# Kernel optimization log

Hardware: AMD Instinct MI355X
Metric: run time of the kernel (lower is better)

The kernel has to match this reference:

```python
import jax, jax.numpy as jnp
import numpy as np


def _prelu(x, a):
    return jnp.where(x >= 0, x, a * x)


def _conv1x1(x, w, b, a):
    # x: [N,C,H,W], w: [O,C], b: [O] -> PReLU(conv1x1(x))
    y = jnp.einsum('oc,nchw->nohw', w, x) + b[None, :, None, None]
    return _prelu(y, a)


def setup_inputs() -> dict:
    key = jax.random.key(0)
    ks = jax.random.split(key, 8)
    N, C, H, W = 4, 128, 64, 64
    Cr = C // 2  # reduction=2
    sC = 1.0 / np.sqrt(C)
    x = jax.random.normal(ks[0], (N, C, H, W), dtype=jnp.float32)
    w1 = jax.random.normal(ks[1], (Cr, C), dtype=jnp.float32) * sC
    b1 = jnp.zeros((Cr,), dtype=jnp.float32)
    a1 = jnp.asarray(0.25, dtype=jnp.float32)  # PReLU (single shared slope)
    w2 = jax.random.normal(ks[2], (Cr, C), dtype=jnp.float32) * sC
    b2 = jnp.zeros((Cr,), dtype=jnp.float32)
    a2 = jnp.asarray(0.25, dtype=jnp.float32)
    wa = jax.random.normal(ks[3], (C, C), dtype=jnp.float32) * sC
    ba = jnp.zeros((C,), dtype=jnp.float32)
    aa = jnp.asarray(0.25, dtype=jnp.float32)
    return {"x": x, "w1": w1, "b1": b1, "a1": a1,
            "w2": w2, "b2": b2, "a2": a2,
            "wa": wa, "ba": ba, "aa": aa}


def reference(x, w1, b1, a1, w2, b2, a2, wa, ba, aa):
    N, C, H, W = x.shape
    HW = H * W
    e1 = _conv1x1(x, w1, b1, a1).reshape(N, -1, HW)   # [N,Cr,HW]
    e2 = _conv1x1(x, w2, b2, a2).reshape(N, -1, HW)   # [N,Cr,HW]
    asm = _conv1x1(x, wa, ba, aa).reshape(N, C, HW)   # [N,C,HW]
    # ksize=1: per-channel outer products summed over channels == single contraction
    score = jnp.einsum('nci,ncj->nij', e1, e2)        # [N,HW,HW]
    score = jax.nn.softmax(score, axis=2)
    out = jnp.einsum('nij,ncj->nci', score, asm)      # [N,C,HW]
    return out.reshape(N, C, H, W)
```

## Files before the change

### kernel.cpp

```cpp
#include <hip/hip_runtime.h>
#include <hip/hip_bf16.h>
#include <stdint.h>


typedef float   f32x16 __attribute__((ext_vector_type(16)));
typedef __bf16  bf16x8 __attribute__((ext_vector_type(8)));
typedef __bf16  bf16x2 __attribute__((ext_vector_type(2)));
typedef unsigned int u32x4 __attribute__((ext_vector_type(4)));
typedef unsigned int u32x2 __attribute__((ext_vector_type(2)));

#define L2E 1.4426950408889634f
#define NSHIFT (-12.0f * L2E)

#define Q_OFF   (0u)
#define K_OFF   (2u << 20)
#define V_OFF   (4u << 20)
#define DEN_OFF (8u << 20)
#define XTH_OFF ((8u << 20) + (1u << 19))
#define XTL_OFF (XTH_OFF + (4u << 20))
#define WH_OFF  (XTL_OFF + (4u << 20))
#define WL_OFF  (WH_OFF + (1u << 16))
#define OP_OFF  XTH_OFF

__device__ inline unsigned short f2bf(float f) {
  unsigned u = __builtin_bit_cast(unsigned, f);
  return (unsigned short)((u + 0x7FFFu + ((u >> 16) & 1u)) >> 16);
}
__device__ inline float bf2f(unsigned short h) {
  unsigned u = ((unsigned)h) << 16;
  return __builtin_bit_cast(float, u);
}

__device__ inline void gld_lds16(const void* g, void* l) {
  __builtin_amdgcn_global_load_lds(
      (const __attribute__((address_space(1))) unsigned*)g,
      (__attribute__((address_space(3))) unsigned*)l, 16, 0, 0);
}

__global__ __launch_bounds__(256) void transpose_kernel(
    const float* __restrict__ x, char* __restrict__ ws) {
  int bid = blockIdx.x;
  int n = bid >> 7, rem = bid & 127;
  int c0 = (rem >> 6) * 64, s0 = (rem & 63) * 64;
  int tid = threadIdx.x;
  __shared__ float tl[64][65];
  const float* xb = x + (size_t)n * 128 * 4096;
#pragma unroll
  for (int i = 0; i < 16; ++i) {
    int cl = (tid >> 6) * 16 + i;
    tl[cl][tid & 63] = xb[(size_t)(c0 + cl) * 4096 + s0 + (tid & 63)];
  }
  __syncthreads();
  char* XH = ws + XTH_OFF + (size_t)n * (4096 * 256);
  char* XL = ws + XTL_OFF + (size_t)n * (4096 * 256);
#pragma unroll
  for (int it = 0; it < 2; ++it) {
    int sl = (tid >> 3) + it * 32;
    int c8 = (tid & 7) * 8;
    unsigned short uh[8], ul[8];
#pragma unroll
    for (int i = 0; i < 8; ++i) {
      float v = tl[c8 + i][sl];
      unsigned short h = f2bf(v);
      uh[i] = h;
      ul[i] = f2bf(v - bf2f(h));
    }
    u32x4 ph, pl;
    ph.x = ((unsigned)uh[1] << 16) | uh[0]; ph.y = ((unsigned)uh[3] << 16) | uh[2];
    ph.z = ((unsigned)uh[5] << 16) | uh[4]; ph.w = ((unsigned)uh[7] << 16) | uh[6];
    pl.x = ((unsigned)ul[1] << 16) | ul[0]; pl.y = ((unsigned)ul[3] << 16) | ul[2];
    pl.z = ((unsigned)ul[5] << 16) | ul[4]; pl.w = ((unsigned)ul[7] << 16) | ul[6];
    size_t off = (size_t)(s0 + sl) * 256 + c0 * 2 + (tid & 7) * 16;
    *(u32x4*)(XH + off) = ph;
    *(u32x4*)(XL + off) = pl;
  }
}

__global__ void wcast_kernel(const float* __restrict__ w1, const float* __restrict__ w2,
                             const float* __restrict__ wa, char* __restrict__ ws) {
  int idx = blockIdx.x * 256 + threadIdx.x;
  unsigned short* WH = (unsigned short*)(ws + WH_OFF);
  unsigned short* WL = (unsigned short*)(ws + WL_OFF);
#pragma unroll
  for (int r = 0; r < 4; ++r) {
    int i = r * 8192 + idx;
    int oc = i >> 7, c = i & 127;
    float v = oc < 64 ? w1[oc * 128 + c]
            : (oc < 128 ? w2[(oc - 64) * 128 + c] : wa[(oc - 128) * 128 + c]);
    unsigned short h = f2bf(v);
    WH[i] = h;
    WL[i] = f2bf(v - bf2f(h));
  }
}

__global__ __launch_bounds__(256) void conv_kernel(
    char* __restrict__ ws,
    const float* __restrict__ b1, const float* __restrict__ a1,
    const float* __restrict__ b2, const float* __restrict__ a2,
    const float* __restrict__ ba, const float* __restrict__ aa) {
  int bid = blockIdx.x;
  int n = bid >> 7, st = bid & 127;
  int sb = st * 32;
  int tid = threadIdx.x;
  int wid = tid >> 6, lane = tid & 63, l31 = lane & 31, hi = lane >> 5;
  const char* XH = ws + XTH_OFF + (size_t)n * (4096 * 256);
  const char* XL = ws + XTL_OFF + (size_t)n * (4096 * 256);
  const char* WH = ws + WH_OFF;
  const char* WL = ws + WL_OFF;
  int oc0 = wid * 64;

  f32x16 acc[2];
  acc[0] = 0.f; acc[1] = 0.f;
#pragma unroll
  for (int c0 = 0; c0 < 8; ++c0) {
    size_t xo = (size_t)(sb + l31) * 256 + c0 * 32 + hi * 16;
    bf16x8 xh = *(const bf16x8*)(XH + xo);
    bf16x8 xl = *(const bf16x8*)(XL + xo);
#pragma unroll
    for (int mb = 0; mb < 2; ++mb) {
      size_t wo = (size_t)(oc0 + mb * 32 + l31) * 256 + c0 * 32 + hi * 16;
      bf16x8 wh = *(const bf16x8*)(WH + wo);
      bf16x8 wl = *(const bf16x8*)(WL + wo);
      acc[mb] = __builtin_amdgcn_mfma_f32_32x32x16_bf16(wh, xh, acc[mb], 0, 0, 0);
      acc[mb] = __builtin_amdgcn_mfma_f32_32x32x16_bf16(wh, xl, acc[mb], 0, 0, 0);
      acc[mb] = __builtin_amdgcn_mfma_f32_32x32x16_bf16(wl, xh, acc[mb], 0, 0, 0);
    }
  }

  __shared__ float tl[2][64][33];
  char* Qw = ws + Q_OFF + (size_t)n * (4096 * 64 * 2);
  char* Kw = ws + K_OFF + (size_t)n * (4096 * 64 * 2);
  unsigned short* Vw = (unsigned short*)(ws + V_OFF) + (size_t)n * 128 * 4096;

  if (wid < 2) {
    const float* bb = wid ? b2 : b1;
    float slope = wid ? a2[0] : a1[0];
#pragma unroll
    for (int mb = 0; mb < 2; ++mb)
#pragma unroll
      for (int reg = 0; reg < 16; ++reg) {
        int row = mb * 32 + (reg & 3) + 8 * (reg >> 2) + 4 * hi;
        float y = acc[mb][reg] + bb[row];
        y = fmaxf(y, 0.f) + slope * fminf(y, 0.f);
        tl[wid][row][l31] = y;
      }
  } else {
    float slope = aa[0];
#pragma unroll
    for (int mb = 0; mb < 2; ++mb)
#pragma unroll
      for (int reg = 0; reg < 16; ++reg) {
        int dv = (wid - 2) * 64 + mb * 32 + (reg & 3) + 8 * (reg >> 2) + 4 * hi;
        float y = acc[mb][reg] + ba[dv];
        y = fmaxf(y, 0.f) + slope * fminf(y, 0.f);
        Vw[(size_t)dv * 4096 + sb + l31] = f2bf(y);
      }
  }
  __syncthreads();
  if (wid < 2) {
    char* Og = wid ? Kw : Qw;
#pragma unroll
    for (int it = 0; it < 4; ++it) {
      int sl = (lane >> 3) + it * 8;
      unsigned short u[8];
#pragma unroll
      for (int i = 0; i < 8; ++i) u[i] = f2bf(tl[wid][(lane & 7) * 8 + i][sl]);
      u32x4 pv;
      pv.x = ((unsigned)u[1] << 16) | u[0]; pv.y = ((unsigned)u[3] << 16) | u[2];
      pv.z = ((unsigned)u[5] << 16) | u[4]; pv.w = ((unsigned)u[7] << 16) | u[6];
      *(u32x4*)(Og + (size_t)(sb + sl) * 128 + (lane & 7) * 16) = pv;
    }
  }
}

__global__ __launch_bounds__(256, 2) void attn_kernel(char* __restrict__ ws) {
  int bid = blockIdx.x;
  int batch   = (bid >> 1) & 3;
  int quarter = (bid >> 3) & 3;
  int qtile   = ((bid >> 5) << 1) | (bid & 1);
  int tid = threadIdx.x;
  int wid = tid >> 6, lane = tid & 63, l31 = lane & 31, hi = lane >> 5;

  const char* Qb = ws + Q_OFF + (size_t)batch * (4096 * 64 * 2);
  const char* Kb = ws + K_OFF + (size_t)batch * (4096 * 64 * 2);
  const char* Vb = ws + V_OFF + (size_t)batch * (128 * 4096 * 2);

  __shared__ char kbuf[2][64 * 128];
  __shared__ char vbuf[2][128 * 128];

  int q0 = qtile * 128 + wid * 32;

  bf16x8 qf[4];
#pragma unroll
  for (int d0 = 0; d0 < 4; ++d0)
    qf[d0] = *(const bf16x8*)(Qb + (size_t)(q0 + l31) * 128 + d0 * 32 + hi * 16);

  f32x16 oacc[4];
#pragma unroll
  for (int i = 0; i < 4; ++i) oacc[i] = 0.f;
  float den = 0.f;

  int t0 = quarter * 16;

  auto stage = [&](int b, int tile) {
    int kv0 = tile * 64;
#pragma unroll
    for (int i = 0; i < 2; ++i) {
      int base = wid * 2048 + i * 1024;
      int L = base + (lane << 4);
      int r = L >> 7, sl = (L >> 4) & 7;
      const char* src = Kb + (size_t)(kv0 + r) * 128 + ((sl ^ (r & 7)) << 4);
      gld_lds16(src, &kbuf[b][base]);
    }
#pragma unroll
    for (int i = 0; i < 4; ++i) {
      int base = wid * 4096 + i * 1024;
      int L = base + (lane << 4);
      int r = L >> 7, sl = (L >> 4) & 7;
      const char* src = Vb + (size_t)r * 8192 + kv0 * 2 + ((sl ^ (r & 7)) << 4);
      gld_lds16(src, &vbuf[b][base]);
    }
  };

  stage(0, t0);
  __syncthreads();
  int cur = 0;

  for (int t = 0; t < 16; ++t) {
    if (t + 1 < 16) stage(cur ^ 1, t0 + t + 1);

    f32x16 sacc[2];
    sacc[0] = 0.f; sacc[1] = 0.f;
#pragma unroll
    for (int kb = 0; kb < 2; ++kb) {
      int r = kb * 32 + l31;
#pragma unroll
      for (int d0 = 0; d0 < 4; ++d0) {
        bf16x8 kf = *(const bf16x8*)(&kbuf[cur][r * 128 + (((d0 * 2 + hi) ^ (r & 7)) << 4)]);
        sacc[kb] = __builtin_amdgcn_mfma_f32_32x32x16_bf16(kf, qf[d0], sacc[kb], 0, 0, 0);
      }
    }

    float p[2][16];
#pragma unroll
    for (int kb = 0; kb < 2; ++kb)
#pragma unroll
      for (int i = 0; i < 16; ++i) {
        float e = exp2f(fmaf(sacc[kb][i], L2E, NSHIFT));
        p[kb][i] = e;
        den += e;
      }

    unsigned pk[2][8];
#pragma unroll
    for (int kb = 0; kb < 2; ++kb)
#pragma unroll
      for (int m = 0; m < 8; ++m) {
        bf16x2 bp = { (__bf16)p[kb][2 * m], (__bf16)p[kb][2 * m + 1] };
        pk[kb][m] = __builtin_bit_cast(unsigned, bp);
      }

#pragma unroll
    for (int kc = 0; kc < 4; ++kc) {
      const int kb = kc >> 1, bs = (kc & 1) * 4;
      u32x2 r0 = __builtin_amdgcn_permlane32_swap(pk[kb][bs + 0], pk[kb][bs + 2],
                                                  false, false);
      u32x2 r1 = __builtin_amdgcn_permlane32_swap(pk[kb][bs + 1], pk[kb][bs + 3],
                                                  false, false);
      u32x4 pu = {r0.x, r1.x, r0.y, r1.y};
      bf16x8 pf = __builtin_bit_cast(bf16x8, pu);
#pragma unroll
      for (int dvb = 0; dvb < 4; ++dvb) {
        int r = dvb * 32 + l31;
        bf16x8 vf = *(const bf16x8*)(&vbuf[cur][r * 128 + (((kc * 2 + hi) ^ (r & 7)) << 4)]);
        oacc[dvb] = __builtin_amdgcn_mfma_f32_32x32x16_bf16(vf, pf, oacc[dvb], 0, 0, 0);
      }
    }

    __syncthreads();
    cur ^= 1;
  }

  float* OP = (float*)(ws + OP_OFF) +
              (size_t)((batch * 32 + qtile) * 4 + quarter) * 128 * 128;
  int qloc = wid * 32 + l31;
#pragma unroll
  for (int dvb = 0; dvb < 4; ++dvb)
#pragma unroll
    for (int reg = 0; reg < 16; ++reg) {
      int dv = dvb * 32 + (reg & 3) + 8 * (reg >> 2) + 4 * hi;
      OP[dv * 128 + qloc] = oacc[dvb][reg];
    }
  float dtot = den + __shfl_xor(den, 32, 64);
  if (hi == 0) {
    float* DEN = (float*)(ws + DEN_OFF) +
                 (size_t)((batch * 32 + qtile) * 4 + quarter) * 128;
    DEN[qloc] = dtot;
  }
}

__global__ __launch_bounds__(256) void combine_kernel(const char* __restrict__ ws,
                                                      float* __restrict__ out) {
  int idx = blockIdx.x * 256 + threadIdx.x;
  int n = idx >> 19;
  int dv = (idx >> 12) & 127;
  int s = idx & 4095;
  int qt = s >> 7, ql = s & 127;
  const float* OP = (const float*)(ws + OP_OFF);
  const float* DEN = (const float*)(ws + DEN_OFF);
  size_t pb = (size_t)((n * 32 + qt) * 4);
  float num = 0.f, den = 0.f;
#pragma unroll
  for (int h = 0; h < 4; ++h) {
    num += OP[((pb + h) * 128 + dv) * 128 + ql];
    den += DEN[(pb + h) * 128 + ql];
  }
  out[idx] = num / den;
}

extern "C" void kernel_launch(void* const* d_in, const int* in_sizes, int n_in,
                              void* d_out, int out_size, void* d_ws, size_t ws_size,
                              hipStream_t stream) {
  (void)in_sizes; (void)n_in; (void)out_size; (void)ws_size;
  const float* x  = (const float*)d_in[0];
  const float* w1 = (const float*)d_in[1];
  const float* b1 = (const float*)d_in[2];
  const float* a1 = (const float*)d_in[3];
  const float* w2 = (const float*)d_in[4];
  const float* b2 = (const float*)d_in[5];
  const float* a2 = (const float*)d_in[6];
  const float* wa = (const float*)d_in[7];
  const float* ba = (const float*)d_in[8];
  const float* aa = (const float*)d_in[9];
  char* ws = (char*)d_ws;
  float* out = (float*)d_out;

  transpose_kernel<<<dim3(512), dim3(256), 0, stream>>>(x, ws);
  wcast_kernel<<<dim3(32), dim3(256), 0, stream>>>(w1, w2, wa, ws);
  conv_kernel<<<dim3(512), dim3(256), 0, stream>>>(ws, b1, a1, b2, a2, ba, aa);
  attn_kernel<<<dim3(512), dim3(256), 0, stream>>>(ws);
  combine_kernel<<<dim3(8192), dim3(256), 0, stream>>>(ws, out);
}
```

Baseline: 73.20 us.

## Fuse transpose into conv, split attention KV eightways, drop softmax shift

Removes the separate transpose kernel: the conv kernel now loads x tiles into LDS and does the bf16 hi/lo split inline. The log2(e) scale is folded into Q during conv, so the attention kernel can use raw exp2 with no fixed shift. Attention is split into 8 KV chunks over 1024 blocks with occupancy hint 3, s_setprio around MFMA groups, and bf16 partial outputs that the combine kernel sums. This cuts launches, intermediate traffic and exp work, but loses the overflow guard from the shift and stores partial outputs at bf16 precision.

```diff
diff --git a/kernel.cpp b/kernel.cpp
--- a/kernel.cpp
+++ b/kernel.cpp
@@ -10,17 +10,14 @@
 typedef unsigned int u32x2 __attribute__((ext_vector_type(2)));
 
 #define L2E 1.4426950408889634f
-#define NSHIFT (-12.0f * L2E)
 
 #define Q_OFF   (0u)
 #define K_OFF   (2u << 20)
 #define V_OFF   (4u << 20)
 #define DEN_OFF (8u << 20)
-#define XTH_OFF ((8u << 20) + (1u << 19))
-#define XTL_OFF (XTH_OFF + (4u << 20))
-#define WH_OFF  (XTL_OFF + (4u << 20))
+#define WH_OFF  ((8u << 20) + (1u << 19))
 #define WL_OFF  (WH_OFF + (1u << 16))
-#define OP_OFF  XTH_OFF
+#define OP_OFF  (9u << 20)
 
 __device__ inline unsigned short f2bf(float f) {
   unsigned u = __builtin_bit_cast(unsigned, f);
@@ -35,45 +32,6 @@
   __builtin_amdgcn_global_load_lds(
       (const __attribute__((address_space(1))) unsigned*)g,
       (__attribute__((address_space(3))) unsigned*)l, 16, 0, 0);
-}
-
-__global__ __launch_bounds__(256) void transpose_kernel(
-    const float* __restrict__ x, char* __restrict__ ws) {
-  int bid = blockIdx.x;
-  int n = bid >> 7, rem = bid & 127;
-  int c0 = (rem >> 6) * 64, s0 = (rem & 63) * 64;
-  int tid = threadIdx.x;
-  __shared__ float tl[64][65];
-  const float* xb = x + (size_t)n * 128 * 4096;
-#pragma unroll
-  for (int i = 0; i < 16; ++i) {
-    int cl = (tid >> 6) * 16 + i;
-    tl[cl][tid & 63] = xb[(size_t)(c0 + cl) * 4096 + s0 + (tid & 63)];
-  }
-  __syncthreads();
-  char* XH = ws + XTH_OFF + (size_t)n * (4096 * 256);
-  char* XL = ws + XTL_OFF + (size_t)n * (4096 * 256);
-#pragma unroll
-  for (int it = 0; it < 2; ++it) {
-    int sl = (tid >> 3) + it * 32;
-    int c8 = (tid & 7) * 8;
-    unsigned short uh[8], ul[8];
-#pragma unroll
-    for (int i = 0; i < 8; ++i) {
-      float v = tl[c8 + i][sl];
-      unsigned short h = f2bf(v);
-      uh[i] = h;
-      ul[i] = f2bf(v - bf2f(h));
-    }
-    u32x4 ph, pl;
-    ph.x = ((unsigned)uh[1] << 16) | uh[0]; ph.y = ((unsigned)uh[3] << 16) | uh[2];
-    ph.z = ((unsigned)uh[5] << 16) | uh[4]; ph.w = ((unsigned)uh[7] << 16) | uh[6];
-    pl.x = ((unsigned)ul[1] << 16) | ul[0]; pl.y = ((unsigned)ul[3] << 16) | ul[2];
-    pl.z = ((unsigned)ul[5] << 16) | ul[4]; pl.w = ((unsigned)ul[7] << 16) | ul[6];
-    size_t off = (size_t)(s0 + sl) * 256 + c0 * 2 + (tid & 7) * 16;
-    *(u32x4*)(XH + off) = ph;
-    *(u32x4*)(XL + off) = pl;
-  }
 }
 
 __global__ void wcast_kernel(const float* __restrict__ w1, const float* __restrict__ w2,
@@ -94,7 +52,7 @@
 }
 
 __global__ __launch_bounds__(256) void conv_kernel(
-    char* __restrict__ ws,
+    const float* __restrict__ x, char* __restrict__ ws,
     const float* __restrict__ b1, const float* __restrict__ a1,
     const float* __restrict__ b2, const float* __restrict__ a2,
     const float* __restrict__ ba, const float* __restrict__ aa) {
@@ -103,8 +61,20 @@
   int sb = st * 32;
   int tid = threadIdx.x;
   int wid = tid >> 6, lane = tid & 63, l31 = lane & 31, hi = lane >> 5;
-  const char* XH = ws + XTH_OFF + (size_t)n * (4096 * 256);
-  const char* XL = ws + XTL_OFF + (size_t)n * (4096 * 256);
+
+  __shared__ float xl[128][36];
+  __shared__ float tl[2][64][33];
+
+  const float* xb = x + (size_t)n * 128 * 4096;
+#pragma unroll
+  for (int it = 0; it < 4; ++it) {
+    int flat4 = tid + 256 * it;
+    int c = flat4 >> 3, s4 = flat4 & 7;
+    float4 v = *(const float4*)(xb + (size_t)c * 4096 + sb + s4 * 4);
+    *(float4*)&xl[c][s4 * 4] = v;
+  }
+  __syncthreads();
+
   const char* WH = ws + WH_OFF;
   const char* WL = ws + WL_OFF;
   int oc0 = wid * 64;
@@ -113,21 +83,27 @@
   acc[0] = 0.f; acc[1] = 0.f;
 #pragma unroll
   for (int c0 = 0; c0 < 8; ++c0) {
-    size_t xo = (size_t)(sb + l31) * 256 + c0 * 32 + hi * 16;
-    bf16x8 xh = *(const bf16x8*)(XH + xo);
-    bf16x8 xl = *(const bf16x8*)(XL + xo);
+    __bf16 eh[8], el[8];
+#pragma unroll
+    for (int j = 0; j < 8; ++j) {
+      float v = xl[c0 * 16 + hi * 8 + j][l31];
+      __bf16 h = (__bf16)v;
+      eh[j] = h;
+      el[j] = (__bf16)(v - (float)h);
+    }
+    bf16x8 xh = {eh[0], eh[1], eh[2], eh[3], eh[4], eh[5], eh[6], eh[7]};
+    bf16x8 xlo = {el[0], el[1], el[2], el[3], el[4], el[5], el[6], el[7]};
 #pragma unroll
     for (int mb = 0; mb < 2; ++mb) {
       size_t wo = (size_t)(oc0 + mb * 32 + l31) * 256 + c0 * 32 + hi * 16;
       bf16x8 wh = *(const bf16x8*)(WH + wo);
       bf16x8 wl = *(const bf16x8*)(WL + wo);
       acc[mb] = __builtin_amdgcn_mfma_f32_32x32x16_bf16(wh, xh, acc[mb], 0, 0, 0);
-      acc[mb] = __builtin_amdgcn_mfma_f32_32x32x16_bf16(wh, xl, acc[mb], 0, 0, 0);
+      acc[mb] = __builtin_amdgcn_mfma_f32_32x32x16_bf16(wh, xlo, acc[mb], 0, 0, 0);
       acc[mb] = __builtin_amdgcn_mfma_f32_32x32x16_bf16(wl, xh, acc[mb], 0, 0, 0);
     }
   }
 
-  __shared__ float tl[2][64][33];
   char* Qw = ws + Q_OFF + (size_t)n * (4096 * 64 * 2);
   char* Kw = ws + K_OFF + (size_t)n * (4096 * 64 * 2);
   unsigned short* Vw = (unsigned short*)(ws + V_OFF) + (size_t)n * 128 * 4096;
@@ -135,6 +111,7 @@
   if (wid < 2) {
     const float* bb = wid ? b2 : b1;
     float slope = wid ? a2[0] : a1[0];
+    float scl = wid ? 1.0f : L2E;
 #pragma unroll
     for (int mb = 0; mb < 2; ++mb)
 #pragma unroll
@@ -142,7 +119,7 @@
         int row = mb * 32 + (reg & 3) + 8 * (reg >> 2) + 4 * hi;
         float y = acc[mb][reg] + bb[row];
         y = fmaxf(y, 0.f) + slope * fminf(y, 0.f);
-        tl[wid][row][l31] = y;
+        tl[wid][row][l31] = y * scl;
       }
   } else {
     float slope = aa[0];
@@ -173,11 +150,11 @@
   }
 }
 
-__global__ __launch_bounds__(256, 2) void attn_kernel(char* __restrict__ ws) {
+__global__ __launch_bounds__(256, 3) void attn_kernel(char* __restrict__ ws) {
   int bid = blockIdx.x;
-  int batch   = (bid >> 1) & 3;
-  int quarter = (bid >> 3) & 3;
-  int qtile   = ((bid >> 5) << 1) | (bid & 1);
+  int split = bid & 7;
+  int qt = (bid >> 3) & 31;
+  int batch = bid >> 8;
   int tid = threadIdx.x;
   int wid = tid >> 6, lane = tid & 63, l31 = lane & 31, hi = lane >> 5;
 
@@ -188,7 +165,7 @@
   __shared__ char kbuf[2][64 * 128];
   __shared__ char vbuf[2][128 * 128];
 
-  int q0 = qtile * 128 + wid * 32;
+  int q0 = qt * 128 + wid * 32;
 
   bf16x8 qf[4];
 #pragma unroll
@@ -200,7 +177,7 @@
   for (int i = 0; i < 4; ++i) oacc[i] = 0.f;
   float den = 0.f;
 
-  int t0 = quarter * 16;
+  int t0 = split * 8;
 
   auto stage = [&](int b, int tile) {
     int kv0 = tile * 64;
@@ -226,37 +203,34 @@
   __syncthreads();
   int cur = 0;
 
-  for (int t = 0; t < 16; ++t) {
-    if (t + 1 < 16) stage(cur ^ 1, t0 + t + 1);
+  for (int t = 0; t < 8; ++t) {
+    if (t + 1 < 8) stage(cur ^ 1, t0 + t + 1);
 
     f32x16 sacc[2];
     sacc[0] = 0.f; sacc[1] = 0.f;
+    __builtin_amdgcn_s_setprio(1);
 #pragma unroll
     for (int kb = 0; kb < 2; ++kb) {
       int r = kb * 32 + l31;
 #pragma unroll
       for (int d0 = 0; d0 < 4; ++d0) {
-        bf16x8 kf = *(const bf16x8*)(&kbuf[cur][r * 128 + (((d0 * 2 + hi) ^ (r & 7)) << 4)]);
-        sacc[kb] = __builtin_amdgcn_mfma_f32_32x32x16_bf16(kf, qf[d0], sacc[kb], 0, 0, 0);
-      }
-    }
-
-    float p[2][16];
+        bf16x8 kf = *(const bf16x8*)(
+            &kbuf[cur][r * 128 + (((d0 * 2 + hi) ^ (r & 7)) << 4)]);
+        sacc[kb] = __builtin_amdgcn_mfma_f32_32x32x16_bf16(kf, qf[d0],
+                                                           sacc[kb], 0, 0, 0);
+      }
+    }
+    __builtin_amdgcn_s_setprio(0);
+
+    unsigned pk[2][8];
 #pragma unroll
     for (int kb = 0; kb < 2; ++kb)
 #pragma unroll
-      for (int i = 0; i < 16; ++i) {
-        float e = exp2f(fmaf(sacc[kb][i], L2E, NSHIFT));
-        p[kb][i] = e;
-        den += e;
-      }
-
-    unsigned pk[2][8];
-#pragma unroll
-    for (int kb = 0; kb < 2; ++kb)
-#pragma unroll
       for (int m = 0; m < 8; ++m) {
-        bf16x2 bp = { (__bf16)p[kb][2 * m], (__bf16)p[kb][2 * m + 1] };
+        float e0 = __builtin_amdgcn_exp2f(sacc[kb][2 * m]);
+        float e1 = __builtin_amdgcn_exp2f(sacc[kb][2 * m + 1]);
+        den += e0 + e1;
+        bf16x2 bp = { (__bf16)e0, (__bf16)e1 };
         pk[kb][m] = __builtin_bit_cast(unsigned, bp);
       }
 
@@ -269,32 +243,36 @@
                                                   false, false);
       u32x4 pu = {r0.x, r1.x, r0.y, r1.y};
       bf16x8 pf = __builtin_bit_cast(bf16x8, pu);
+      __builtin_amdgcn_s_setprio(1);
 #pragma unroll
       for (int dvb = 0; dvb < 4; ++dvb) {
         int r = dvb * 32 + l31;
-        bf16x8 vf = *(const bf16x8*)(&vbuf[cur][r * 128 + (((kc * 2 + hi) ^ (r & 7)) << 4)]);
-        oacc[dvb] = __builtin_amdgcn_mfma_f32_32x32x16_bf16(vf, pf, oacc[dvb], 0, 0, 0);
-      }
+        bf16x8 vf = *(const bf16x8*)(
+            &vbuf[cur][r * 128 + (((kc * 2 + hi) ^ (r & 7)) << 4)]);
+        oacc[dvb] = __builtin_amdgcn_mfma_f32_32x32x16_bf16(vf, pf,
+                                                            oacc[dvb], 0, 0, 0);
+      }
+      __builtin_amdgcn_s_setprio(0);
     }
 
     __syncthreads();
     cur ^= 1;
   }
 
-  float* OP = (float*)(ws + OP_OFF) +
-              (size_t)((batch * 32 + qtile) * 4 + quarter) * 128 * 128;
+  unsigned short* OPu = (unsigned short*)(ws + OP_OFF) +
+                        (size_t)((batch * 32 + qt) * 8 + split) * 128 * 128;
   int qloc = wid * 32 + l31;
 #pragma unroll
   for (int dvb = 0; dvb < 4; ++dvb)
 #pragma unroll
     for (int reg = 0; reg < 16; ++reg) {
       int dv = dvb * 32 + (reg & 3) + 8 * (reg >> 2) + 4 * hi;
-      OP[dv * 128 + qloc] = oacc[dvb][reg];
+      OPu[dv * 128 + qloc] = f2bf(oacc[dvb][reg]);
     }
   float dtot = den + __shfl_xor(den, 32, 64);
   if (hi == 0) {
     float* DEN = (float*)(ws + DEN_OFF) +
-                 (size_t)((batch * 32 + qtile) * 4 + quarter) * 128;
+                 (size_t)((batch * 32 + qt) * 8 + split) * 128;
     DEN[qloc] = dtot;
   }
 }
@@ -306,13 +284,13 @@
   int dv = (idx >> 12) & 127;
   int s = idx & 4095;
   int qt = s >> 7, ql = s & 127;
-  const float* OP = (const float*)(ws + OP_OFF);
+  const unsigned short* OPu = (const unsigned short*)(ws + OP_OFF);
   const float* DEN = (const float*)(ws + DEN_OFF);
-  size_t pb = (size_t)((n * 32 + qt) * 4);
+  size_t pb = (size_t)((n * 32 + qt) * 8);
   float num = 0.f, den = 0.f;
 #pragma unroll
-  for (int h = 0; h < 4; ++h) {
-    num += OP[((pb + h) * 128 + dv) * 128 + ql];
+  for (int h = 0; h < 8; ++h) {
+    num += bf2f(OPu[(pb + h) * 16384 + (size_t)dv * 128 + ql]);
     den += DEN[(pb + h) * 128 + ql];
   }
   out[idx] = num / den;
@@ -335,9 +313,8 @@
   char* ws = (char*)d_ws;
   float* out = (float*)d_out;
 
-  transpose_kernel<<<dim3(512), dim3(256), 0, stream>>>(x, ws);
   wcast_kernel<<<dim3(32), dim3(256), 0, stream>>>(w1, w2, wa, ws);
-  conv_kernel<<<dim3(512), dim3(256), 0, stream>>>(ws, b1, a1, b2, a2, ba, aa);
-  attn_kernel<<<dim3(512), dim3(256), 0, stream>>>(ws);
+  conv_kernel<<<dim3(512), dim3(256), 0, stream>>>(x, ws, b1, a1, b2, a2, ba, aa);
+  attn_kernel<<<dim3(1024), dim3(256), 0, stream>>>(ws);
   combine_kernel<<<dim3(8192), dim3(256), 0, stream>>>(ws, out);
 }
```

Result: faster. 64.65 us (-11.7%).
